# Optimization experiments

Measured on AMD Instinct MI355X. Metric: run time of the kernel, lower is better.

## Reference

```python
import jax, jax.numpy as jnp
import numpy as np

B, N = 16, 16          # batch, boxes per image
H, W = 640, 640        # image size
PH, PW = 300, 300      # learned patch size
MIN_AREA = 60.0
MAX_ANG = 20.0 * np.pi / 180.0


def setup_inputs() -> dict:
    key = jax.random.key(0)
    k1, k2, k3 = jax.random.split(key, 3)
    images = jax.random.uniform(k1, (B, H, W, 3), jnp.float32, -1.0, 1.0)
    patch = jax.random.uniform(k2, (PH, PW, 3), jnp.float32, -1.0, 1.0)
    kb1, kb2, kb3 = jax.random.split(k3, 3)
    ymin = jax.random.uniform(kb1, (B, N), jnp.float32, 0.0, H - 220.0)
    xmin = jax.random.uniform(kb2, (B, N), jnp.float32, 0.0, W - 220.0)
    hw = jax.random.uniform(kb3, (B, N, 2), jnp.float32, 100.0, 200.0)
    boxes = jnp.stack([ymin, xmin, ymin + hw[..., 0], xmin + hw[..., 1]], axis=-1)
    scale = jnp.float32(0.4)
    return {"boxes": boxes, "images": images, "patch": patch, "scale": scale}


def _bilinear(img, ys, xs):
    # img [Ph,Pw,3]; ys,xs [H,W] continuous source coords -> [H,W,3]
    Ph, Pw = img.shape[0], img.shape[1]
    y0 = jnp.floor(ys)
    x0 = jnp.floor(xs)
    wy = (ys - y0)[..., None]
    wx = (xs - x0)[..., None]
    y0i = jnp.clip(y0.astype(jnp.int32), 0, Ph - 1)
    y1i = jnp.clip(y0i + 1, 0, Ph - 1)
    x0i = jnp.clip(x0.astype(jnp.int32), 0, Pw - 1)
    x1i = jnp.clip(x0i + 1, 0, Pw - 1)
    v00 = img[y0i, x0i]
    v01 = img[y0i, x1i]
    v10 = img[y1i, x0i]
    v11 = img[y1i, x1i]
    return v00 * (1 - wy) * (1 - wx) + v01 * (1 - wy) * wx + v10 * wy * (1 - wx) + v11 * wy * wx


def _per_image(img, boxes_i, patch, scale, key):
    # random_print_adjust: per-channel affine jitter of the patch
    kw, kb, kloop = jax.random.split(key, 3)
    w = jax.random.normal(kw, (1, 1, 3), jnp.float32) * 0.1 + 0.5
    b = jax.random.normal(kb, (1, 1, 3), jnp.float32) * 0.01
    p = jnp.clip(w * patch + b, -1.0, 1.0)
    # BrightnessMatcher: shift patch mean brightness to match the image
    p = jnp.clip(p + (jnp.mean(img) - jnp.mean(p)), -1.0, 1.0)

    oimg = img
    mask0 = jnp.zeros_like(img)
    yy, xx = jnp.meshgrid(jnp.arange(H, dtype=jnp.float32),
                          jnp.arange(W, dtype=jnp.float32), indexing="ij")

    def step(carry, inp):
        image, mask = carry
        box, kk = inp
        ymin, xmin, ymax, xmax = box[0], box[1], box[2], box[3]
        h = ymax - ymin
        ww = xmax - xmin
        longer = jnp.maximum(h, ww)
        ps = jnp.floor(longer * scale)                       # patch_h == patch_w
        diag = jnp.minimum(jnp.sqrt(2.0).astype(jnp.float32) * ps, jnp.float32(W))
        oy = ymin + h / 2.0
        ox = xmin + ww / 2.0
        y0 = jnp.maximum(oy - diag / 2.0, 0.0)
        x0 = jnp.maximum(ox - diag / 2.0, 0.0)
        y0 = jnp.where(y0 + diag > H, H - diag, y0)
        x0 = jnp.where(x0 + diag > W, W - diag, x0)
        # int casts as in the TF code (values are >= 0, trunc == floor)
        y0i = jnp.floor(y0)
        x0i = jnp.floor(x0)
        phi = jnp.maximum(jnp.floor(ps), 1.0)
        diagi = jnp.floor(diag)
        valid_box = (phi * phi) > MIN_AREA

        k1, k2, k3 = jax.random.split(kk, 3)
        angle = jax.random.uniform(k1, (), jnp.float32, -MAX_ANG, MAX_ANG)

        # inverse warp: output pixel -> padded-patch coords -> resized-patch coords
        u = yy - y0i
        v = xx - x0i
        in_sq = (u >= 0) & (v >= 0) & (u < diagi) & (v < diagi)
        c = (diagi - 1.0) / 2.0
        ca, sa = jnp.cos(angle), jnp.sin(angle)
        su = c + ca * (u - c) - sa * (v - c)
        sv = c + sa * (u - c) + ca * (v - c)
        top = jnp.floor((diagi - phi) / 2.0)   # pad offset (floor top/left)
        py = su - top
        px = sv - top
        valid_src = (py >= 0) & (py <= phi - 1) & (px >= 0) & (px <= phi - 1)
        # resized-patch coords -> original patch coords (bilinear resize, half-pixel)
        sy = (py + 0.5) * (PH / phi) - 0.5
        sx = (px + 0.5) * (PW / phi) - 0.5
        samp = _bilinear(p, sy, sx)                                   # [H,W,3]
        noise = jax.random.uniform(k2, samp.shape, jnp.float32, -0.1, 0.1)
        bright = jax.random.uniform(k3, (), jnp.float32, -0.3, 0.3)
        im = jnp.clip(samp + noise + bright, -1.0, 1.0)
        val = jnp.where(valid_src[..., None], im, -2.0)
        val = jnp.where(val < -1.0, image, val)   # fill with current background
        val = jnp.clip(val, -1.0, 1.0)
        sel = (in_sq & valid_box)[..., None]
        new_image = jnp.where(sel, val, image)
        new_mask = jnp.where(sel, oimg - val, mask)
        return (new_image, new_mask), None

    keys = jax.random.split(kloop, N)
    (img_out, mask_out), _ = jax.lax.scan(step, (img, mask0), (boxes_i, keys))
    return img_out, mask_out


def reference(boxes, images, patch, scale):
    keys = jax.random.split(jax.random.key(42), B)
    img_out, mask_out = jax.vmap(_per_image, in_axes=(0, 0, None, None, 0))(
        images, boxes, patch, scale, keys)
    return img_out, mask_out
```

## Files before the change

kernel.cpp:

```cpp
#include <hip/hip_runtime.h>
#include <stdint.h>
#include <math.h>

#define B_ 16
#define N_ 16
#define H_ 640
#define W_ 640
#define PH_ 300
#define PW_ 300

#define IMG_ELEMS (H_*W_*3)
#define PATCH_ELEMS (PH_*PW_*3)

__device__ __forceinline__ uint2 tf2x32(uint32_t k0, uint32_t k1, uint32_t x0, uint32_t x1) {
  uint32_t k2 = k0 ^ k1 ^ 0x1BD11BDAu;
#define TFR(r) x0 += x1; x1 = (x1 << (r)) | (x1 >> (32 - (r))); x1 ^= x0;
  x0 += k0; x1 += k1;
  TFR(13) TFR(15) TFR(26) TFR(6)
  x0 += k1; x1 += k2 + 1u;
  TFR(17) TFR(29) TFR(16) TFR(24)
  x0 += k2; x1 += k0 + 2u;
  TFR(13) TFR(15) TFR(26) TFR(6)
  x0 += k0; x1 += k1 + 3u;
  TFR(17) TFR(29) TFR(16) TFR(24)
  x0 += k1; x1 += k2 + 4u;
  TFR(13) TFR(15) TFR(26) TFR(6)
  x0 += k2; x1 += k0 + 5u;
#undef TFR
  return make_uint2(x0, x1);
}

__device__ __forceinline__ uint32_t rb32(uint32_t k0, uint32_t k1, uint32_t i) {
  uint2 o = tf2x32(k0, k1, 0u, i);
  return o.x ^ o.y;
}

__device__ __forceinline__ float u01f(uint32_t bits) {
  return __uint_as_float((bits >> 9) | 0x3F800000u) - 1.0f;
}

__device__ __forceinline__ float erfinv32(float x) {
  float w = -log1pf(-x * x);
  float p;
  if (w < 5.0f) {
    w = w - 2.5f;
    p = 2.81022636e-08f;
    p = fmaf(p, w, 3.43273939e-07f);
    p = fmaf(p, w, -3.5233877e-06f);
    p = fmaf(p, w, -4.39150654e-06f);
    p = fmaf(p, w, 0.00021858087f);
    p = fmaf(p, w, -0.00125372503f);
    p = fmaf(p, w, -0.00417768164f);
    p = fmaf(p, w, 0.246640727f);
    p = fmaf(p, w, 1.50140941f);
  } else {
    w = sqrtf(w) - 3.0f;
    p = -0.000200214257f;
    p = fmaf(p, w, 0.000100950558f);
    p = fmaf(p, w, 0.00134934322f);
    p = fmaf(p, w, -0.00367342844f);
    p = fmaf(p, w, 0.00573950773f);
    p = fmaf(p, w, -0.0076224613f);
    p = fmaf(p, w, 0.00943887047f);
    p = fmaf(p, w, 1.00167406f);
    p = fmaf(p, w, 2.83297682f);
  }
  return p * x;
}

__device__ __forceinline__ float jnormal(uint32_t bits) {
  float lo = __uint_as_float(0xBF7FFFFFu);
  float span = 1.0f - lo;
  float u = fmaxf(lo, u01f(bits) * span + lo);
  return 1.4142135623730951f * erfinv32(u);
}

__global__ void setup_kernel(const float* __restrict__ boxes, const float* __restrict__ scale_p,
                             float* __restrict__ params, float* __restrict__ wb) {
  int t = threadIdx.x;
  if (t >= B_*N_) return;
  int b = t >> 4, n = t & 15;
  uint2 kb = tf2x32(0u, 42u, 0u, (uint32_t)b);
  uint2 kw  = tf2x32(kb.x, kb.y, 0u, 0u);
  uint2 kbk = tf2x32(kb.x, kb.y, 0u, 1u);
  uint2 kl  = tf2x32(kb.x, kb.y, 0u, 2u);
  if (n == 0) {
    wb[b*8+0] = jnormal(rb32(kw.x,  kw.y,  0u)) * 0.1f + 0.5f;
    wb[b*8+1] = jnormal(rb32(kw.x,  kw.y,  1u)) * 0.1f + 0.5f;
    wb[b*8+2] = jnormal(rb32(kw.x,  kw.y,  2u)) * 0.1f + 0.5f;
    wb[b*8+3] = jnormal(rb32(kbk.x, kbk.y, 0u)) * 0.01f;
    wb[b*8+4] = jnormal(rb32(kbk.x, kbk.y, 1u)) * 0.01f;
    wb[b*8+5] = jnormal(rb32(kbk.x, kbk.y, 2u)) * 0.01f;
  }
  uint2 kk = tf2x32(kl.x, kl.y, 0u, (uint32_t)n);
  uint2 k1 = tf2x32(kk.x, kk.y, 0u, 0u);
  uint2 k2 = tf2x32(kk.x, kk.y, 0u, 1u);
  uint2 k3 = tf2x32(kk.x, kk.y, 0u, 2u);
  const float MA = (float)(20.0 * 3.14159265358979323846 / 180.0);
  float angle  = fmaxf(-MA,   u01f(rb32(k1.x, k1.y, 0u)) * (MA - (-MA)) + (-MA));
  float bright = fmaxf(-0.3f, u01f(rb32(k3.x, k3.y, 0u)) * (0.3f - (-0.3f)) + (-0.3f));

  const float* bx = boxes + (size_t)t * 4;
  float ymin = bx[0], xmin = bx[1], ymax = bx[2], xmax = bx[3];
  float sc = scale_p[0];
  float h = ymax - ymin, ww = xmax - xmin;
  float longer = fmaxf(h, ww);
  float ps = floorf(longer * sc);
  float diag = fminf(sqrtf(2.0f) * ps, (float)W_);
  float oy = ymin + h * 0.5f;
  float ox = xmin + ww * 0.5f;
  float y0 = fmaxf(oy - diag * 0.5f, 0.0f);
  float x0 = fmaxf(ox - diag * 0.5f, 0.0f);
  if (y0 + diag > (float)H_) y0 = (float)H_ - diag;
  if (x0 + diag > (float)W_) x0 = (float)W_ - diag;
  float y0i = floorf(y0), x0i = floorf(x0);
  float phi = fmaxf(floorf(ps), 1.0f);
  float diagi = floorf(diag);
  float validf = ((phi * phi) > 60.0f) ? 1.0f : 0.0f;
  float c = (diagi - 1.0f) * 0.5f;
  float top = floorf((diagi - phi) * 0.5f);

  float* P = params + t * 16;
  P[0] = y0i; P[1] = x0i; P[2] = diagi; P[3] = phi;
  P[4] = c;
  P[5] = (float)cos((double)angle);
  P[6] = (float)sin((double)angle);
  P[7] = top;
  P[8] = bright; P[9] = (float)PH_ / phi; P[10] = 0.0f; P[11] = validf;
  P[12] = __uint_as_float(k2.x); P[13] = __uint_as_float(k2.y); P[14] = 0.0f; P[15] = 0.0f;
}

__global__ __launch_bounds__(256) void reduce_kernel(
    const float* __restrict__ images, const float* __restrict__ patch,
    const float* __restrict__ wb, double* __restrict__ partials) {
  int b = blockIdx.y, j = blockIdx.x, t = threadIdx.x;
  const float* img = images + (size_t)b * IMG_ELEMS;
  double s = 0.0;
  for (int i = j * 256 + t; i < IMG_ELEMS; i += 64 * 256) s += (double)img[i];
  float w0 = wb[b*8+0], w1 = wb[b*8+1], w2 = wb[b*8+2];
  float b0 = wb[b*8+3], b1 = wb[b*8+4], b2 = wb[b*8+5];
  double sp = 0.0;
  for (int i = j * 256 + t; i < PATCH_ELEMS; i += 64 * 256) {
    int q = i / 3; int ch = i - q * 3;
    float wv = (ch == 0) ? w0 : ((ch == 1) ? w1 : w2);
    float bv = (ch == 0) ? b0 : ((ch == 1) ? b1 : b2);
    float pv = fminf(fmaxf(wv * patch[i] + bv, -1.0f), 1.0f);
    sp += (double)pv;
  }
  __shared__ double sh[256];
  sh[t] = s; __syncthreads();
  for (int o = 128; o > 0; o >>= 1) { if (t < o) sh[t] += sh[t + o]; __syncthreads(); }
  if (t == 0) partials[((size_t)b * 64 + j) * 2 + 0] = sh[0];
  __syncthreads();
  sh[t] = sp; __syncthreads();
  for (int o = 128; o > 0; o >>= 1) { if (t < o) sh[t] += sh[t + o]; __syncthreads(); }
  if (t == 0) partials[((size_t)b * 64 + j) * 2 + 1] = sh[0];
}

__global__ __launch_bounds__(256) void main_kernel(
    const float* __restrict__ images, const float* __restrict__ patch,
    const float* __restrict__ params, const float* __restrict__ wb,
    const double* __restrict__ partials, float* __restrict__ out) {
  __shared__ float sP[N_ * 16];
  __shared__ float sWB[6];
  __shared__ float sD;
  __shared__ int sList[N_];
  __shared__ int sCount;
  __shared__ double sRi[64], sRp[64];

  int b = blockIdx.y;
  int tid = threadIdx.x;
  if (tid < N_ * 16) sP[tid] = params[b * N_ * 16 + tid];
  if (tid < 6) sWB[tid] = wb[b * 8 + tid];
  if (tid < 64) {
    sRi[tid] = partials[((size_t)b * 64 + tid) * 2 + 0];
    sRp[tid] = partials[((size_t)b * 64 + tid) * 2 + 1];
  }
  __syncthreads();
  if (tid == 0) {
    double si = 0.0, sp = 0.0;
    for (int j = 0; j < 64; j++) { si += sRi[j]; sp += sRp[j]; }
    float mi = (float)(si / (double)IMG_ELEMS);
    float mp = (float)(sp / (double)PATCH_ELEMS);
    sD = mi - mp;
    int pblk = blockIdx.x * 1024;
    int ys = pblk / W_;
    int ye = (pblk + 1023) / W_;
    int cnt = 0;
    for (int n = 0; n < N_; n++) {
      const float* P = sP + n * 16;
      if (P[11] == 0.0f) continue;
      float fy0 = P[0];
      float fy1 = P[0] + P[2] - 1.0f;
      if (fy1 < (float)ys || fy0 > (float)ye) continue;
      sList[cnt++] = n;
    }
    sCount = cnt;
  }
  __syncthreads();

  int lane = tid & 63;
  int wv   = tid >> 6;
  int span = blockIdx.x * 1024 + wv * 256;
  size_t ibase = (size_t)b * (H_ * W_) * 3;

  int   pj[4];  float yfj[4], xfj[4];
#pragma unroll
  for (int j = 0; j < 4; j++) {
    int p = span + j * 64 + lane;
    int chunk = span + j * 64;
    int y = chunk / W_;
    pj[j]  = p;
    yfj[j] = (float)y;
    xfj[j] = (float)(chunk - y * W_ + lane);
  }

  float orig[12], img[12], mk[12];
#pragma unroll
  for (int j = 0; j < 4; j++) {
    const float* src = images + ibase + (size_t)pj[j] * 3;
    orig[j*3+0] = src[0]; orig[j*3+1] = src[1]; orig[j*3+2] = src[2];
  }
#pragma unroll
  for (int e = 0; e < 12; e++) { img[e] = orig[e]; mk[e] = 0.0f; }

  float dsh = sD;
  int cnt = sCount;
  for (int li = 0; li < cnt; li++) {
    const float* P = sP + sList[li] * 16;
    float P0 = P[0], P1 = P[1], diagi = P[2];
    float phi = P[3], c = P[4], ca = P[5], sa = P[6], top = P[7], bright = P[8], sph = P[9];
    uint32_t k2a = __float_as_uint(P[12]);
    uint32_t k2b = __float_as_uint(P[13]);
#pragma unroll
    for (int j = 0; j < 4; j++) {
      float u = yfj[j] - P0;
      if (!(u >= 0.0f && u < diagi)) continue;
      float v = xfj[j] - P1;
      if (!(v >= 0.0f && v < diagi)) continue;
      float t1 = u - c, t2 = v - c;
      float su = (c + ca * t1) - sa * t2;
      float sv = (c + sa * t1) + ca * t2;
      float py = su - top;
      float px = sv - top;
      bool vsrc = (py >= 0.0f) && (py <= phi - 1.0f) && (px >= 0.0f) && (px <= phi - 1.0f);
      if (vsrc) {
        float sy = (py + 0.5f) * sph - 0.5f;
        float sx = (px + 0.5f) * sph - 0.5f;
        float fy = floorf(sy), fx = floorf(sx);
        float wy = sy - fy, wxv = sx - fx;
        int iy0 = min(max((int)fy, 0), PH_ - 1);
        int iy1 = min(iy0 + 1, PH_ - 1);
        int ix0 = min(max((int)fx, 0), PW_ - 1);
        int ix1 = min(ix0 + 1, PW_ - 1);
        int o00 = (iy0 * PW_ + ix0) * 3;
        int o01 = (iy0 * PW_ + ix1) * 3;
        int o10 = (iy1 * PW_ + ix0) * 3;
        int o11 = (iy1 * PW_ + ix1) * 3;
        float omwy = 1.0f - wy, omwx = 1.0f - wxv;
        int nbase = pj[j] * 3;
#pragma unroll
        for (int ch = 0; ch < 3; ch++) {
          float wv2 = sWB[ch], bv = sWB[3 + ch];
          float a00 = fminf(fmaxf(wv2 * patch[o00 + ch] + bv, -1.0f), 1.0f);
          float a01 = fminf(fmaxf(wv2 * patch[o01 + ch] + bv, -1.0f), 1.0f);
          float a10 = fminf(fmaxf(wv2 * patch[o10 + ch] + bv, -1.0f), 1.0f);
          float a11 = fminf(fmaxf(wv2 * patch[o11 + ch] + bv, -1.0f), 1.0f);
          a00 = fminf(fmaxf(a00 + dsh, -1.0f), 1.0f);
          a01 = fminf(fmaxf(a01 + dsh, -1.0f), 1.0f);
          a10 = fminf(fmaxf(a10 + dsh, -1.0f), 1.0f);
          a11 = fminf(fmaxf(a11 + dsh, -1.0f), 1.0f);
          float samp = ((a00 * omwy) * omwx) + ((a01 * omwy) * wxv)
                     + ((a10 * wy) * omwx) + ((a11 * wy) * wxv);
          int i = nbase + ch;
          uint32_t bits = rb32(k2a, k2b, (uint32_t)i);
          float nz = fmaxf(-0.1f, u01f(bits) * (0.1f - (-0.1f)) + (-0.1f));
          float imv = fminf(fmaxf((samp + nz) + bright, -1.0f), 1.0f);
          img[j * 3 + ch] = imv;
          mk[j * 3 + ch] = orig[j * 3 + ch] - imv;
        }
      } else {
#pragma unroll
        for (int ch = 0; ch < 3; ch++) mk[j * 3 + ch] = orig[j * 3 + ch] - img[j * 3 + ch];
      }
    }
  }

  size_t moff = (size_t)B_ * (H_ * W_) * 3;
#pragma unroll
  for (int j = 0; j < 4; j++) {
    float* od = out + ibase + (size_t)pj[j] * 3;
    float* md = od + moff;
#pragma unroll
    for (int ch = 0; ch < 3; ch++) {
      __builtin_nontemporal_store(img[j*3+ch], od + ch);
      __builtin_nontemporal_store(mk[j*3+ch],  md + ch);
    }
  }
}

extern "C" void kernel_launch(void* const* d_in, const int* in_sizes, int n_in,
                              void* d_out, int out_size, void* d_ws, size_t ws_size,
                              hipStream_t stream) {
  const float* boxes  = (const float*)d_in[0];
  const float* images = (const float*)d_in[1];
  const float* patch  = (const float*)d_in[2];
  const float* scale  = (const float*)d_in[3];
  float* out = (float*)d_out;

  float* params = (float*)d_ws;
  float* wb     = params + B_ * N_ * 16;
  double* partials = (double*)((char*)d_ws + 20480);

  setup_kernel<<<1, 256, 0, stream>>>(boxes, scale, params, wb);
  reduce_kernel<<<dim3(64, B_), 256, 0, stream>>>(images, patch, wb, partials);
  main_kernel<<<dim3((H_ * W_) / 1024, B_), 256, 0, stream>>>(images, patch, params, wb, partials, out);
}
```

Measured before the change: 294.7 us.

## Precompute adjusted patch per image and remap blocks for XCD locality

Adds a finalize kernel that computes the per-image brightness shift once, and a patch_adjust kernel that writes a fully adjusted (affine, clamped, shifted) patch per image to workspace. The main kernel then gathers pre-adjusted values instead of redoing the affine, clamp and shift on every bilinear tap. It also flattens the grid and interleaves batch indices across block IDs, and uses nontemporal loads for the image. In exchange it adds two extra launches and about 17 MB of adjusted-patch storage that must be written and then gathered, and it falls back to the old path if the workspace is too small.

```diff
diff --git a/kernel.cpp b/kernel.cpp
--- a/kernel.cpp
+++ b/kernel.cpp
@@ -11,6 +11,8 @@
 
 #define IMG_ELEMS (H_*W_*3)
 #define PATCH_ELEMS (PH_*PW_*3)
+
+typedef float f32x4 __attribute__((ext_vector_type(4)));
 
 __device__ __forceinline__ uint2 tf2x32(uint32_t k0, uint32_t k1, uint32_t x0, uint32_t x1) {
   uint32_t k2 = k0 ^ k1 ^ 0x1BD11BDAu;
@@ -157,38 +159,71 @@
   if (t == 0) partials[((size_t)b * 64 + j) * 2 + 1] = sh[0];
 }
 
+__global__ void finalize_kernel(const double* __restrict__ partials, float* __restrict__ dvals) {
+  int t = threadIdx.x;
+  if (t < B_) {
+    double si = 0.0, sp = 0.0;
+    for (int j = 0; j < 64; j++) {
+      si += partials[((size_t)t * 64 + j) * 2 + 0];
+      sp += partials[((size_t)t * 64 + j) * 2 + 1];
+    }
+    float mi = (float)(si / (double)IMG_ELEMS);
+    float mp = (float)(sp / (double)PATCH_ELEMS);
+    dvals[t] = mi - mp;
+  }
+}
+
+__global__ __launch_bounds__(256) void patch_adjust_kernel(
+    const float* __restrict__ patch, const float* __restrict__ wb,
+    const float* __restrict__ dvals, float* __restrict__ padj) {
+  int b = blockIdx.y;
+  float w0 = wb[b*8+0], w1 = wb[b*8+1], w2 = wb[b*8+2];
+  float b0 = wb[b*8+3], b1 = wb[b*8+4], b2 = wb[b*8+5];
+  float dsh = dvals[b];
+  float* dst = padj + (size_t)b * PATCH_ELEMS;
+  int i0 = (blockIdx.x * 256 + threadIdx.x) * 4;
+  if (i0 + 3 >= PATCH_ELEMS && i0 >= PATCH_ELEMS) return;
+  if (i0 + 4 <= PATCH_ELEMS) {
+    f32x4 pv = *(const f32x4*)(patch + i0);
+    float o[4];
+#pragma unroll
+    for (int e = 0; e < 4; e++) {
+      int ch = (i0 + e) % 3;
+      float wv = (ch == 0) ? w0 : ((ch == 1) ? w1 : w2);
+      float bv = (ch == 0) ? b0 : ((ch == 1) ? b1 : b2);
+      float a = fminf(fmaxf(wv * pv[e] + bv, -1.0f), 1.0f);
+      o[e] = fminf(fmaxf(a + dsh, -1.0f), 1.0f);
+    }
+    f32x4 ov = {o[0], o[1], o[2], o[3]};
+    *(f32x4*)(dst + i0) = ov;
+  }
+}
+
+template<int PADJ>
 __global__ __launch_bounds__(256) void main_kernel(
-    const float* __restrict__ images, const float* __restrict__ patch,
+    const float* __restrict__ images, const float* __restrict__ patchsrc,
     const float* __restrict__ params, const float* __restrict__ wb,
-    const double* __restrict__ partials, float* __restrict__ out) {
+    const float* __restrict__ dvals, float* __restrict__ out) {
   __shared__ float sP[N_ * 16];
   __shared__ float sWB[6];
-  __shared__ float sD;
   __shared__ int sList[N_];
   __shared__ int sCount;
-  __shared__ double sRi[64], sRp[64];
-
-  int b = blockIdx.y;
+
+  int bid = blockIdx.x;
+  int b  = (bid & 7) * 2 + ((bid >> 3) & 1);
+  int pb = bid >> 4;
   int tid = threadIdx.x;
+
   if (tid < N_ * 16) sP[tid] = params[b * N_ * 16 + tid];
-  if (tid < 6) sWB[tid] = wb[b * 8 + tid];
-  if (tid < 64) {
-    sRi[tid] = partials[((size_t)b * 64 + tid) * 2 + 0];
-    sRp[tid] = partials[((size_t)b * 64 + tid) * 2 + 1];
-  }
-  __syncthreads();
+  if (PADJ == 0 && tid < 6) sWB[tid] = wb[b * 8 + tid];
   if (tid == 0) {
-    double si = 0.0, sp = 0.0;
-    for (int j = 0; j < 64; j++) { si += sRi[j]; sp += sRp[j]; }
-    float mi = (float)(si / (double)IMG_ELEMS);
-    float mp = (float)(sp / (double)PATCH_ELEMS);
-    sD = mi - mp;
-    int pblk = blockIdx.x * 1024;
+    const float* Pb = params + b * N_ * 16;
+    int pblk = pb * 1024;
     int ys = pblk / W_;
     int ye = (pblk + 1023) / W_;
     int cnt = 0;
     for (int n = 0; n < N_; n++) {
-      const float* P = sP + n * 16;
+      const float* P = Pb + n * 16;
       if (P[11] == 0.0f) continue;
       float fy0 = P[0];
       float fy1 = P[0] + P[2] - 1.0f;
@@ -201,8 +236,10 @@
 
   int lane = tid & 63;
   int wv   = tid >> 6;
-  int span = blockIdx.x * 1024 + wv * 256;
+  int span = pb * 1024 + wv * 256;
   size_t ibase = (size_t)b * (H_ * W_) * 3;
+  const float* patchb = PADJ ? (patchsrc + (size_t)b * PATCH_ELEMS) : patchsrc;
+  float dsh = PADJ ? 0.0f : dvals[b];
 
   int   pj[4];  float yfj[4], xfj[4];
 #pragma unroll
@@ -219,12 +256,13 @@
 #pragma unroll
   for (int j = 0; j < 4; j++) {
     const float* src = images + ibase + (size_t)pj[j] * 3;
-    orig[j*3+0] = src[0]; orig[j*3+1] = src[1]; orig[j*3+2] = src[2];
+    orig[j*3+0] = __builtin_nontemporal_load(src + 0);
+    orig[j*3+1] = __builtin_nontemporal_load(src + 1);
+    orig[j*3+2] = __builtin_nontemporal_load(src + 2);
   }
 #pragma unroll
   for (int e = 0; e < 12; e++) { img[e] = orig[e]; mk[e] = 0.0f; }
 
-  float dsh = sD;
   int cnt = sCount;
   for (int li = 0; li < cnt; li++) {
     const float* P = sP + sList[li] * 16;
@@ -261,15 +299,23 @@
         int nbase = pj[j] * 3;
 #pragma unroll
         for (int ch = 0; ch < 3; ch++) {
-          float wv2 = sWB[ch], bv = sWB[3 + ch];
-          float a00 = fminf(fmaxf(wv2 * patch[o00 + ch] + bv, -1.0f), 1.0f);
-          float a01 = fminf(fmaxf(wv2 * patch[o01 + ch] + bv, -1.0f), 1.0f);
-          float a10 = fminf(fmaxf(wv2 * patch[o10 + ch] + bv, -1.0f), 1.0f);
-          float a11 = fminf(fmaxf(wv2 * patch[o11 + ch] + bv, -1.0f), 1.0f);
-          a00 = fminf(fmaxf(a00 + dsh, -1.0f), 1.0f);
-          a01 = fminf(fmaxf(a01 + dsh, -1.0f), 1.0f);
-          a10 = fminf(fmaxf(a10 + dsh, -1.0f), 1.0f);
-          a11 = fminf(fmaxf(a11 + dsh, -1.0f), 1.0f);
+          float a00, a01, a10, a11;
+          if (PADJ) {
+            a00 = patchb[o00 + ch];
+            a01 = patchb[o01 + ch];
+            a10 = patchb[o10 + ch];
+            a11 = patchb[o11 + ch];
+          } else {
+            float wv2 = sWB[ch], bv = sWB[3 + ch];
+            a00 = fminf(fmaxf(wv2 * patchb[o00 + ch] + bv, -1.0f), 1.0f);
+            a01 = fminf(fmaxf(wv2 * patchb[o01 + ch] + bv, -1.0f), 1.0f);
+            a10 = fminf(fmaxf(wv2 * patchb[o10 + ch] + bv, -1.0f), 1.0f);
+            a11 = fminf(fmaxf(wv2 * patchb[o11 + ch] + bv, -1.0f), 1.0f);
+            a00 = fminf(fmaxf(a00 + dsh, -1.0f), 1.0f);
+            a01 = fminf(fmaxf(a01 + dsh, -1.0f), 1.0f);
+            a10 = fminf(fmaxf(a10 + dsh, -1.0f), 1.0f);
+            a11 = fminf(fmaxf(a11 + dsh, -1.0f), 1.0f);
+          }
           float samp = ((a00 * omwy) * omwx) + ((a01 * omwy) * wxv)
                      + ((a10 * wy) * omwx) + ((a11 * wy) * wxv);
           int i = nbase + ch;
@@ -310,9 +356,21 @@
 
   float* params = (float*)d_ws;
   float* wb     = params + B_ * N_ * 16;
+  float* dvals  = wb + B_ * 8;
   double* partials = (double*)((char*)d_ws + 20480);
+  float* padj   = (float*)((char*)d_ws + 36864);
+  const size_t PADJ_NEED = 36864 + (size_t)B_ * PATCH_ELEMS * 4;
 
   setup_kernel<<<1, 256, 0, stream>>>(boxes, scale, params, wb);
   reduce_kernel<<<dim3(64, B_), 256, 0, stream>>>(images, patch, wb, partials);
-  main_kernel<<<dim3((H_ * W_) / 1024, B_), 256, 0, stream>>>(images, patch, params, wb, partials, out);
-}
+  finalize_kernel<<<1, 64, 0, stream>>>(partials, dvals);
+  if (ws_size >= PADJ_NEED) {
+    patch_adjust_kernel<<<dim3((PATCH_ELEMS + 1023) / 1024, B_), 256, 0, stream>>>(
+        patch, wb, dvals, padj);
+    main_kernel<1><<<(H_ * W_ * B_) / 1024, 256, 0, stream>>>(
+        images, padj, params, wb, dvals, out);
+  } else {
+    main_kernel<0><<<(H_ * W_ * B_) / 1024, 256, 0, stream>>>(
+        images, patch, params, wb, dvals, out);
+  }
+}
```

New measurement: 298.1 us. Within noise of the previous version (+1.2%).
